# Kernel tuning notes

Hardware: AMD Instinct MI355X
Metric: run time of the kernel (lower is better)

The kernel has to match this reference:

```python
import jax, jax.numpy as jnp
import numpy as np

N = 100000
E = 1600000
F_IN = 128
DIM = 32
C = 2
BN_EPS = 1e-5


def setup_inputs() -> dict:
    key = jax.random.key(0)
    ks = jax.random.split(key, 24)
    s = 0.1
    inp = {
        'x': jax.random.normal(ks[0], (N, F_IN), dtype=jnp.float32),
        'edge_index': jax.random.randint(ks[1], (2, E), 0, N, dtype=jnp.int64),
        'edge_attr': jax.random.normal(ks[2], (E, 1), dtype=jnp.float32),
        'batch': jnp.zeros((N,), dtype=jnp.int64),
        # GIN layer 1 MLP: Linear(F_IN, DIM) -> ReLU -> Linear(DIM, DIM)
        'w1a': jax.random.normal(ks[3], (F_IN, DIM), dtype=jnp.float32) * s,
        'b1a': jnp.zeros((DIM,), dtype=jnp.float32),
        'w1b': jax.random.normal(ks[4], (DIM, DIM), dtype=jnp.float32) * s,
        'b1b': jnp.zeros((DIM,), dtype=jnp.float32),
        'g1': jnp.ones((DIM,), dtype=jnp.float32),
        'be1': jnp.zeros((DIM,), dtype=jnp.float32),
        # GIN layer 2
        'w2a': jax.random.normal(ks[5], (DIM, DIM), dtype=jnp.float32) * s,
        'b2a': jnp.zeros((DIM,), dtype=jnp.float32),
        'w2b': jax.random.normal(ks[6], (DIM, DIM), dtype=jnp.float32) * s,
        'b2b': jnp.zeros((DIM,), dtype=jnp.float32),
        'g2': jnp.ones((DIM,), dtype=jnp.float32),
        'be2': jnp.zeros((DIM,), dtype=jnp.float32),
        # GIN layer 3
        'w3a': jax.random.normal(ks[7], (DIM, DIM), dtype=jnp.float32) * s,
        'b3a': jnp.zeros((DIM,), dtype=jnp.float32),
        'w3b': jax.random.normal(ks[8], (DIM, DIM), dtype=jnp.float32) * s,
        'b3b': jnp.zeros((DIM,), dtype=jnp.float32),
        'g3': jnp.ones((DIM,), dtype=jnp.float32),
        'be3': jnp.zeros((DIM,), dtype=jnp.float32),
        # head
        'fw1': jax.random.normal(ks[9], (DIM, DIM), dtype=jnp.float32) * s,
        'fb1': jnp.zeros((DIM,), dtype=jnp.float32),
        'fw2': jax.random.normal(ks[10], (DIM, C), dtype=jnp.float32) * s,
        'fb2': jnp.zeros((C,), dtype=jnp.float32),
    }
    return inp


def _gin(x, src, dst, wa, ba, wb, bb):
    # GINConv with eps=0: h_i = MLP((1+eps)*x_i + sum_{j->i} x_j)
    agg = jax.ops.segment_sum(x[src], dst, num_segments=N)
    h = x + agg
    h = jax.nn.relu(h @ wa + ba) @ wb + bb
    return h


def _bn(h, g, b):
    # BatchNorm1d with batch statistics (training-mode normalization)
    mu = h.mean(axis=0)
    var = h.var(axis=0)  # biased, matches torch normalization
    return (h - mu) * jax.lax.rsqrt(var + BN_EPS) * g + b


def reference(x, edge_index, edge_attr, batch,
              w1a, b1a, w1b, b1b, g1, be1,
              w2a, b2a, w2b, b2b, g2, be2,
              w3a, b3a, w3b, b3b, g3, be3,
              fw1, fb1, fw2, fb2):
    src, dst = edge_index[0], edge_index[1]
    h = _bn(jax.nn.relu(_gin(x, src, dst, w1a, b1a, w1b, b1b)), g1, be1)
    h = _bn(jax.nn.relu(_gin(h, src, dst, w2a, b2a, w2b, b2b)), g2, be2)
    h = _bn(jax.nn.relu(_gin(h, src, dst, w3a, b3a, w3b, b3b)), g3, be3)
    h = jax.nn.relu(h @ fw1 + fb1)
    # dropout treated as identity (eval mode / deterministic reference)
    return h @ fw2 + fb2
```

## Files before the change

kernel.cpp:

```cpp
#include <hip/hip_runtime.h>

#define NNODES 100000
#define NEDGES 1600000
#define FIN 128
#define DIM 32
#define BN_EPS 1e-5f
#define NB_TPN ((NNODES + 255) / 256)
#define NBUK ((NNODES + 255) >> 8)
#define CH 8192

__global__ void __launch_bounds__(256) k_proj1(const float* __restrict__ x,
                                               const float* __restrict__ w,
                                               float* __restrict__ z) {
    const int i = blockIdx.x * 256 + threadIdx.x;
    if (i >= NNODES) return;
    const float4* xp = reinterpret_cast<const float4*>(x + (size_t)i * FIN);
    float acc[DIM];
#pragma unroll
    for (int c = 0; c < DIM; ++c) acc[c] = 0.f;

    for (int k0 = 0; k0 < FIN; k0 += 32) {
        float a[32];
        float4 r[8];
#pragma unroll
        for (int q = 0; q < 8; ++q) r[q] = xp[k0 / 4 + q];
#pragma unroll
        for (int q = 0; q < 8; ++q) {
            a[q * 4 + 0] = r[q].x; a[q * 4 + 1] = r[q].y;
            a[q * 4 + 2] = r[q].z; a[q * 4 + 3] = r[q].w;
        }
#pragma unroll
        for (int kk = 0; kk < 32; ++kk) {
            const float tk = a[kk];
#pragma unroll
            for (int c = 0; c < DIM; ++c)
                acc[c] += tk * w[(k0 + kk) * DIM + c];
        }
    }
    float4* zp = reinterpret_cast<float4*>(z + (size_t)i * DIM);
#pragma unroll
    for (int q = 0; q < 8; ++q)
        zp[q] = make_float4(acc[q * 4], acc[q * 4 + 1], acc[q * 4 + 2], acc[q * 4 + 3]);
}

__global__ void k_bhist(const int* __restrict__ ei, int* __restrict__ bucketCnt) {
    __shared__ int cnt[NBUK];
    for (int i = threadIdx.x; i < NBUK; i += 256) cnt[i] = 0;
    __syncthreads();
    const int tid    = blockIdx.x * blockDim.x + threadIdx.x;
    const int stride = gridDim.x * blockDim.x;
    for (int e = tid; e < NEDGES; e += stride)
        atomicAdd(&cnt[ei[NEDGES + e] >> 8], 1);
    __syncthreads();
    for (int i = threadIdx.x; i < NBUK; i += 256)
        if (cnt[i]) atomicAdd(&bucketCnt[i], cnt[i]);
}

__global__ void k_bscan(const int* __restrict__ bucketCnt,
                        int* __restrict__ bbase, int* __restrict__ gcur) {
    __shared__ int sbuf[512];
    const int t = threadIdx.x;
    const int v = (t < NBUK) ? bucketCnt[t] : 0;
    sbuf[t] = v;
    __syncthreads();
    for (int off = 1; off < 512; off <<= 1) {
        const int u = (t >= off) ? sbuf[t - off] : 0;
        __syncthreads();
        sbuf[t] += u;
        __syncthreads();
    }
    if (t < NBUK) { const int ex = sbuf[t] - v; bbase[t] = ex; gcur[t] = ex; }
    if (t == 0) bbase[NBUK] = NEDGES;
}

__global__ void __launch_bounds__(256) k_bscatter(const int* __restrict__ ei,
                                                  int* __restrict__ gcur,
                                                  int2* __restrict__ bucketed) {
    __shared__ int cnt[NBUK];
    __shared__ int base[NBUK];
    const int start = blockIdx.x * CH;
    const int end   = min(start + CH, NEDGES);
    for (int i = threadIdx.x; i < NBUK; i += 256) cnt[i] = 0;
    __syncthreads();
    for (int e = start + threadIdx.x; e < end; e += 256)
        atomicAdd(&cnt[ei[NEDGES + e] >> 8], 1);
    __syncthreads();
    for (int i = threadIdx.x; i < NBUK; i += 256) {
        const int c = cnt[i];
        base[i] = c ? atomicAdd(&gcur[i], c) : 0;
        cnt[i] = 0;
    }
    __syncthreads();
    for (int e = start + threadIdx.x; e < end; e += 256) {
        const int s = ei[e];
        const int d = ei[NEDGES + e];
        const int b = d >> 8;
        const int p = atomicAdd(&cnt[b], 1);
        bucketed[base[b] + p] = make_int2(s, d);
    }
}

__global__ void __launch_bounds__(256) k_bfill(const int2* __restrict__ bucketed,
                                               const int* __restrict__ bbase,
                                               int* __restrict__ rowstart,
                                               int* __restrict__ deg,
                                               int* __restrict__ sorted_src) {
    __shared__ int dcnt[256], dsc[256], cur[256];
    const int b  = blockIdx.x;
    const int lo = bbase[b];
    const int hi = bbase[b + 1];
    const int n0 = b << 8;
    const int t  = threadIdx.x;
    dcnt[t] = 0;
    __syncthreads();
    for (int p = lo + t; p < hi; p += 256)
        atomicAdd(&dcnt[bucketed[p].y - n0], 1);
    __syncthreads();
    const int myc = dcnt[t];
    dsc[t] = myc;
    __syncthreads();
    for (int off = 1; off < 256; off <<= 1) {
        const int u = (t >= off) ? dsc[t - off] : 0;
        __syncthreads();
        dsc[t] += u;
        __syncthreads();
    }
    const int ex = dsc[t] - myc;
    const int node = n0 + t;
    if (node < NNODES) { rowstart[node] = lo + ex; deg[node] = myc; }
    dcnt[t] = ex;
    cur[t] = 0;
    __syncthreads();
    for (int p = lo + t; p < hi; p += 256) {
        const int2 sd = bucketed[p];
        const int dl = sd.y - n0;
        const int pos = atomicAdd(&cur[dl], 1);
        sorted_src[lo + dcnt[dl] + pos] = sd.x;
    }
}

__global__ void k_gather_t(const float* __restrict__ z,
                           const int* __restrict__ rowstart,
                           const int* __restrict__ deg,
                           const int* __restrict__ sorted_src,
                           const float* __restrict__ ba,
                           float* __restrict__ tbuf) {
    const int lane = threadIdx.x & 31;
    const int g    = lane >> 3;
    const int f4   = lane & 7;
    const float4 ba4 = reinterpret_cast<const float4*>(ba)[f4];
    const int hw  = (blockIdx.x * blockDim.x + threadIdx.x) >> 5;
    const int nhw = (gridDim.x * blockDim.x) >> 5;

    for (int i = hw; i < NNODES; i += nhw) {
        const int base = rowstart[i];
        const int cnt  = deg[i];
        float4 agg0 = make_float4(0.f, 0.f, 0.f, 0.f);
        float4 agg1 = make_float4(0.f, 0.f, 0.f, 0.f);
        for (int k0 = 0; k0 < cnt; k0 += 32) {
            int e = 0;
            if (k0 + lane < cnt) e = sorted_src[base + k0 + lane];
            const int m = min(32, cnt - k0);
            for (int j = 0; j < m; j += 8) {
                const int s0 = __shfl(e, j + g, 32);
                const int s1 = __shfl(e, j + 4 + g, 32);
                if (j + g < m) {
                    const float4 zv = *reinterpret_cast<const float4*>(&z[s0 * DIM + f4 * 4]);
                    agg0.x += zv.x; agg0.y += zv.y; agg0.z += zv.z; agg0.w += zv.w;
                }
                if (j + 4 + g < m) {
                    const float4 zv = *reinterpret_cast<const float4*>(&z[s1 * DIM + f4 * 4]);
                    agg1.x += zv.x; agg1.y += zv.y; agg1.z += zv.z; agg1.w += zv.w;
                }
            }
        }
        agg0.x += agg1.x; agg0.y += agg1.y; agg0.z += agg1.z; agg0.w += agg1.w;
#pragma unroll
        for (int mask = 8; mask <= 16; mask <<= 1) {
            agg0.x += __shfl_xor(agg0.x, mask, 32);
            agg0.y += __shfl_xor(agg0.y, mask, 32);
            agg0.z += __shfl_xor(agg0.z, mask, 32);
            agg0.w += __shfl_xor(agg0.w, mask, 32);
        }
        if (g == 0) {
            const float4 zi = *reinterpret_cast<const float4*>(&z[i * DIM + f4 * 4]);
            float4 t;
            t.x = fmaxf(zi.x + agg0.x + ba4.x, 0.f);
            t.y = fmaxf(zi.y + agg0.y + ba4.y, 0.f);
            t.z = fmaxf(zi.z + agg0.z + ba4.z, 0.f);
            t.w = fmaxf(zi.w + agg0.w + ba4.w, 0.f);
            *reinterpret_cast<float4*>(&tbuf[i * DIM + f4 * 4]) = t;
        }
    }
}

__global__ void __launch_bounds__(256) k_mlp2(float* __restrict__ hbuf,
                                              const float* __restrict__ wb,
                                              const float* __restrict__ bb,
                                              float* __restrict__ stats) {
    __shared__ float ssum[DIM], ssq[DIM];
    if (threadIdx.x < DIM) { ssum[threadIdx.x] = 0.f; ssq[threadIdx.x] = 0.f; }
    __syncthreads();

    const int i = blockIdx.x * 256 + threadIdx.x;
    const bool valid = i < NNODES;

    float a[DIM];
    if (valid) {
        const float4* tp = reinterpret_cast<const float4*>(hbuf + (size_t)i * DIM);
        float4 r[8];
#pragma unroll
        for (int q = 0; q < 8; ++q) r[q] = tp[q];
#pragma unroll
        for (int q = 0; q < 8; ++q) {
            a[q * 4 + 0] = r[q].x; a[q * 4 + 1] = r[q].y;
            a[q * 4 + 2] = r[q].z; a[q * 4 + 3] = r[q].w;
        }
    } else {
#pragma unroll
        for (int k = 0; k < DIM; ++k) a[k] = 0.f;
    }

    float acc[DIM];
#pragma unroll
    for (int c = 0; c < DIM; ++c) acc[c] = bb[c];
#pragma unroll
    for (int k = 0; k < DIM; ++k) {
        const float tk = a[k];
#pragma unroll
        for (int c = 0; c < DIM; ++c)
            acc[c] += tk * wb[k * DIM + c];
    }
#pragma unroll
    for (int c = 0; c < DIM; ++c) acc[c] = valid ? fmaxf(acc[c], 0.f) : 0.f;

    if (valid) {
        float4* hp = reinterpret_cast<float4*>(hbuf + (size_t)i * DIM);
#pragma unroll
        for (int q = 0; q < 8; ++q)
            hp[q] = make_float4(acc[q * 4], acc[q * 4 + 1], acc[q * 4 + 2], acc[q * 4 + 3]);
    }

    const int lane = threadIdx.x & 63;
    float lsum = 0.f, lsq = 0.f;
#pragma unroll
    for (int c = 0; c < DIM; ++c) {
        float v  = acc[c];
        float w2 = acc[c] * acc[c];
#pragma unroll
        for (int off = 1; off < 64; off <<= 1) {
            v  += __shfl_xor(v, off);
            w2 += __shfl_xor(w2, off);
        }
        if (lane == c) { lsum = v; lsq = w2; }
    }
    if (lane < DIM) {
        atomicAdd(&ssum[lane], lsum);
        atomicAdd(&ssq[lane], lsq);
    }
    __syncthreads();
    if (threadIdx.x < DIM) {
        atomicAdd(&stats[threadIdx.x],       ssum[threadIdx.x]);
        atomicAdd(&stats[DIM + threadIdx.x], ssq[threadIdx.x]);
    }
}

__global__ void __launch_bounds__(256) k_projbn(const float* __restrict__ h,
                                                const float* __restrict__ stats,
                                                const float* __restrict__ g,
                                                const float* __restrict__ be,
                                                const float* __restrict__ wa,
                                                float* __restrict__ z) {
    const int i = blockIdx.x * 256 + threadIdx.x;
    if (i >= NNODES) return;
    const float4* hp = reinterpret_cast<const float4*>(h + (size_t)i * DIM);
    float a[DIM];
    float4 r[8];
#pragma unroll
    for (int q = 0; q < 8; ++q) r[q] = hp[q];
#pragma unroll
    for (int q = 0; q < 8; ++q) {
        a[q * 4 + 0] = r[q].x; a[q * 4 + 1] = r[q].y;
        a[q * 4 + 2] = r[q].z; a[q * 4 + 3] = r[q].w;
    }
    float acc[DIM];
#pragma unroll
    for (int c = 0; c < DIM; ++c) acc[c] = 0.f;
#pragma unroll
    for (int k = 0; k < DIM; ++k) {
        const float mu  = stats[k] * (1.f / NNODES);
        const float var = stats[DIM + k] * (1.f / NNODES) - mu * mu;
        const float ss  = g[k] * rsqrtf(var + BN_EPS);
        const float st  = be[k] - mu * ss;
        const float tk  = a[k] * ss + st;
#pragma unroll
        for (int c = 0; c < DIM; ++c)
            acc[c] += tk * wa[k * DIM + c];
    }
    float4* zp = reinterpret_cast<float4*>(z + (size_t)i * DIM);
#pragma unroll
    for (int q = 0; q < 8; ++q)
        zp[q] = make_float4(acc[q * 4], acc[q * 4 + 1], acc[q * 4 + 2], acc[q * 4 + 3]);
}

__global__ void __launch_bounds__(256) k_head(const float* __restrict__ h,
                                              const float* __restrict__ stats,
                                              const float* __restrict__ g,
                                              const float* __restrict__ be,
                                              const float* __restrict__ fw1,
                                              const float* __restrict__ fb1,
                                              const float* __restrict__ fw2,
                                              const float* __restrict__ fb2,
                                              float* __restrict__ out) {
    const int i = blockIdx.x * 256 + threadIdx.x;
    if (i >= NNODES) return;
    const float4* hp = reinterpret_cast<const float4*>(h + (size_t)i * DIM);
    float a[DIM];
    float4 r[8];
#pragma unroll
    for (int q = 0; q < 8; ++q) r[q] = hp[q];
#pragma unroll
    for (int q = 0; q < 8; ++q) {
        a[q * 4 + 0] = r[q].x; a[q * 4 + 1] = r[q].y;
        a[q * 4 + 2] = r[q].z; a[q * 4 + 3] = r[q].w;
    }
    float acc[DIM];
#pragma unroll
    for (int c = 0; c < DIM; ++c) acc[c] = fb1[c];
#pragma unroll
    for (int k = 0; k < DIM; ++k) {
        const float mu  = stats[k] * (1.f / NNODES);
        const float var = stats[DIM + k] * (1.f / NNODES) - mu * mu;
        const float ss  = g[k] * rsqrtf(var + BN_EPS);
        const float st  = be[k] - mu * ss;
        const float tk  = a[k] * ss + st;
#pragma unroll
        for (int c = 0; c < DIM; ++c)
            acc[c] += tk * fw1[k * DIM + c];
    }
    float o0 = fb2[0], o1 = fb2[1];
#pragma unroll
    for (int c = 0; c < DIM; ++c) {
        const float u = fmaxf(acc[c], 0.f);
        o0 += u * fw2[c * 2 + 0];
        o1 += u * fw2[c * 2 + 1];
    }
    *reinterpret_cast<float2*>(&out[i * 2]) = make_float2(o0, o1);
}

extern "C" void kernel_launch(void* const* d_in, const int* in_sizes, int n_in,
                              void* d_out, int out_size, void* d_ws, size_t ws_size,
                              hipStream_t stream) {
    const float* x   = (const float*)d_in[0];
    const int*   ei  = (const int*)d_in[1];
    const float* w1a = (const float*)d_in[4];
    const float* b1a = (const float*)d_in[5];
    const float* w1b = (const float*)d_in[6];
    const float* b1b = (const float*)d_in[7];
    const float* g1  = (const float*)d_in[8];
    const float* be1 = (const float*)d_in[9];
    const float* w2a = (const float*)d_in[10];
    const float* b2a = (const float*)d_in[11];
    const float* w2b = (const float*)d_in[12];
    const float* b2b = (const float*)d_in[13];
    const float* g2  = (const float*)d_in[14];
    const float* be2 = (const float*)d_in[15];
    const float* w3a = (const float*)d_in[16];
    const float* b3a = (const float*)d_in[17];
    const float* w3b = (const float*)d_in[18];
    const float* b3b = (const float*)d_in[19];
    const float* g3  = (const float*)d_in[20];
    const float* be3 = (const float*)d_in[21];
    const float* fw1 = (const float*)d_in[22];
    const float* fb1 = (const float*)d_in[23];
    const float* fw2 = (const float*)d_in[24];
    const float* fb2 = (const float*)d_in[25];
    float* out = (float*)d_out;

    float* ws = (float*)d_ws;
    const size_t nf = (size_t)NNODES * DIM;
    float* z     = ws;
    float* h     = ws + nf;
    int2*  bucketed = (int2*)h;
    float* stats = ws + 2 * nf;
    int* rowstart   = (int*)(ws + 2 * nf + 192);
    int* deg        = rowstart + NNODES;
    int* sorted_src = deg + NNODES;
    int* bucketCnt  = sorted_src + NEDGES;
    int* bbase      = bucketCnt + NBUK;
    int* gcur       = bbase + NBUK + 1;

    const int TB = 256, NB_G = 2048;

    hipMemsetAsync(stats, 0, 3 * 64 * sizeof(float), stream);
    hipMemsetAsync(bucketCnt, 0, NBUK * sizeof(int), stream);

    k_bhist<<<512, TB, 0, stream>>>(ei, bucketCnt);
    k_bscan<<<1, 512, 0, stream>>>(bucketCnt, bbase, gcur);
    k_bscatter<<<(NEDGES + CH - 1) / CH, TB, 0, stream>>>(ei, gcur, bucketed);
    k_bfill<<<NBUK, TB, 0, stream>>>(bucketed, bbase, rowstart, deg, sorted_src);

    k_proj1<<<NB_TPN, TB, 0, stream>>>(x, w1a, z);
    k_gather_t<<<NB_G, TB, 0, stream>>>(z, rowstart, deg, sorted_src, b1a, h);
    k_mlp2<<<NB_TPN, TB, 0, stream>>>(h, w1b, b1b, stats + 0);
    k_projbn<<<NB_TPN, TB, 0, stream>>>(h, stats + 0, g1, be1, w2a, z);
    k_gather_t<<<NB_G, TB, 0, stream>>>(z, rowstart, deg, sorted_src, b2a, h);
    k_mlp2<<<NB_TPN, TB, 0, stream>>>(h, w2b, b2b, stats + 64);
    k_projbn<<<NB_TPN, TB, 0, stream>>>(h, stats + 64, g2, be2, w3a, z);
    k_gather_t<<<NB_G, TB, 0, stream>>>(z, rowstart, deg, sorted_src, b3a, h);
    k_mlp2<<<NB_TPN, TB, 0, stream>>>(h, w3b, b3b, stats + 128);
    k_head<<<NB_TPN, TB, 0, stream>>>(h, stats + 128, g3, be3,
                                      fw1, fb1, fw2, fb2, out);
}
```

Baseline: 350.3 us.

## Fuse gather with second MLP layer and BN stats, pack bucketed edges

Merges the neighbor gather kernel and the second linear layer with BN statistics into one kernel. Each half-wavefront computes one output column per lane via shuffles, so the intermediate t buffer is never written to or re-read from global memory. Edge bucketing now packs the source index and the local destination offset into a single int, halving that scratch traffic. The stats memset is folded into the scan kernel, and the per-node kernels move to 64-thread blocks, with proj1 loading the whole input row up front. The packing assumes node ids fit in 17 bits, and the fused kernel does a 32-step shuffle chain for every node.

```diff
diff --git a/kernel.cpp b/kernel.cpp
--- a/kernel.cpp
+++ b/kernel.cpp
@@ -5,36 +5,37 @@
 #define FIN 128
 #define DIM 32
 #define BN_EPS 1e-5f
-#define NB_TPN ((NNODES + 255) / 256)
 #define NBUK ((NNODES + 255) >> 8)
 #define CH 8192
 
-__global__ void __launch_bounds__(256) k_proj1(const float* __restrict__ x,
-                                               const float* __restrict__ w,
-                                               float* __restrict__ z) {
-    const int i = blockIdx.x * 256 + threadIdx.x;
+__global__ void __launch_bounds__(64) k_proj1(const float* __restrict__ x,
+                                              const float* __restrict__ w,
+                                              float* __restrict__ z) {
+    const int i = blockIdx.x * 64 + threadIdx.x;
     if (i >= NNODES) return;
     const float4* xp = reinterpret_cast<const float4*>(x + (size_t)i * FIN);
+    float4 r[32];
+#pragma unroll
+    for (int q = 0; q < 32; ++q) r[q] = xp[q];
+
     float acc[DIM];
 #pragma unroll
     for (int c = 0; c < DIM; ++c) acc[c] = 0.f;
 
-    for (int k0 = 0; k0 < FIN; k0 += 32) {
+#pragma unroll
+    for (int k0 = 0; k0 < 4; ++k0) {
         float a[32];
-        float4 r[8];
-#pragma unroll
-        for (int q = 0; q < 8; ++q) r[q] = xp[k0 / 4 + q];
 #pragma unroll
         for (int q = 0; q < 8; ++q) {
-            a[q * 4 + 0] = r[q].x; a[q * 4 + 1] = r[q].y;
-            a[q * 4 + 2] = r[q].z; a[q * 4 + 3] = r[q].w;
+            a[q * 4 + 0] = r[k0 * 8 + q].x; a[q * 4 + 1] = r[k0 * 8 + q].y;
+            a[q * 4 + 2] = r[k0 * 8 + q].z; a[q * 4 + 3] = r[k0 * 8 + q].w;
         }
 #pragma unroll
         for (int kk = 0; kk < 32; ++kk) {
             const float tk = a[kk];
 #pragma unroll
             for (int c = 0; c < DIM; ++c)
-                acc[c] += tk * w[(k0 + kk) * DIM + c];
+                acc[c] += tk * w[(k0 * 32 + kk) * DIM + c];
         }
     }
     float4* zp = reinterpret_cast<float4*>(z + (size_t)i * DIM);
@@ -57,9 +58,11 @@
 }
 
 __global__ void k_bscan(const int* __restrict__ bucketCnt,
-                        int* __restrict__ bbase, int* __restrict__ gcur) {
+                        int* __restrict__ bbase, int* __restrict__ gcur,
+                        float* __restrict__ stats) {
     __shared__ int sbuf[512];
     const int t = threadIdx.x;
+    if (t < 192) stats[t] = 0.f;
     const int v = (t < NBUK) ? bucketCnt[t] : 0;
     sbuf[t] = v;
     __syncthreads();
@@ -75,7 +78,7 @@
 
 __global__ void __launch_bounds__(256) k_bscatter(const int* __restrict__ ei,
                                                   int* __restrict__ gcur,
-                                                  int2* __restrict__ bucketed) {
+                                                  int* __restrict__ bucketed) {
     __shared__ int cnt[NBUK];
     __shared__ int base[NBUK];
     const int start = blockIdx.x * CH;
@@ -96,11 +99,11 @@
         const int d = ei[NEDGES + e];
         const int b = d >> 8;
         const int p = atomicAdd(&cnt[b], 1);
-        bucketed[base[b] + p] = make_int2(s, d);
-    }
-}
-
-__global__ void __launch_bounds__(256) k_bfill(const int2* __restrict__ bucketed,
+        bucketed[base[b] + p] = s | ((d & 255) << 17);
+    }
+}
+
+__global__ void __launch_bounds__(256) k_bfill(const int* __restrict__ bucketed,
                                                const int* __restrict__ bbase,
                                                int* __restrict__ rowstart,
                                                int* __restrict__ deg,
@@ -109,12 +112,11 @@
     const int b  = blockIdx.x;
     const int lo = bbase[b];
     const int hi = bbase[b + 1];
-    const int n0 = b << 8;
     const int t  = threadIdx.x;
     dcnt[t] = 0;
     __syncthreads();
     for (int p = lo + t; p < hi; p += 256)
-        atomicAdd(&dcnt[bucketed[p].y - n0], 1);
+        atomicAdd(&dcnt[bucketed[p] >> 17], 1);
     __syncthreads();
     const int myc = dcnt[t];
     dsc[t] = myc;
@@ -126,31 +128,44 @@
         __syncthreads();
     }
     const int ex = dsc[t] - myc;
-    const int node = n0 + t;
+    const int node = (b << 8) + t;
     if (node < NNODES) { rowstart[node] = lo + ex; deg[node] = myc; }
     dcnt[t] = ex;
     cur[t] = 0;
     __syncthreads();
     for (int p = lo + t; p < hi; p += 256) {
-        const int2 sd = bucketed[p];
-        const int dl = sd.y - n0;
+        const int v = bucketed[p];
+        const int dl = v >> 17;
         const int pos = atomicAdd(&cur[dl], 1);
-        sorted_src[lo + dcnt[dl] + pos] = sd.x;
-    }
-}
-
-__global__ void k_gather_t(const float* __restrict__ z,
-                           const int* __restrict__ rowstart,
-                           const int* __restrict__ deg,
-                           const int* __restrict__ sorted_src,
-                           const float* __restrict__ ba,
-                           float* __restrict__ tbuf) {
+        sorted_src[lo + dcnt[dl] + pos] = v & 0x1FFFF;
+    }
+}
+
+__global__ void k_gather_mlp(const float* __restrict__ z,
+                             const int* __restrict__ rowstart,
+                             const int* __restrict__ deg,
+                             const int* __restrict__ sorted_src,
+                             const float* __restrict__ ba,
+                             const float* __restrict__ wb,
+                             const float* __restrict__ bb,
+                             float* __restrict__ h,
+                             float* __restrict__ stats) {
+    __shared__ float ssum[DIM], ssq[DIM];
+    if (threadIdx.x < DIM) { ssum[threadIdx.x] = 0.f; ssq[threadIdx.x] = 0.f; }
+    __syncthreads();
+
     const int lane = threadIdx.x & 31;
     const int g    = lane >> 3;
     const int f4   = lane & 7;
     const float4 ba4 = reinterpret_cast<const float4*>(ba)[f4];
+    float wcol[DIM];
+#pragma unroll
+    for (int kk = 0; kk < DIM; ++kk) wcol[kk] = wb[kk * DIM + lane];
+    const float bbl = bb[lane];
+
     const int hw  = (blockIdx.x * blockDim.x + threadIdx.x) >> 5;
     const int nhw = (gridDim.x * blockDim.x) >> 5;
+    float lsum = 0.f, lsq = 0.f;
 
     for (int i = hw; i < NNODES; i += nhw) {
         const int base = rowstart[i];
@@ -182,82 +197,31 @@
             agg0.z += __shfl_xor(agg0.z, mask, 32);
             agg0.w += __shfl_xor(agg0.w, mask, 32);
         }
-        if (g == 0) {
-            const float4 zi = *reinterpret_cast<const float4*>(&z[i * DIM + f4 * 4]);
-            float4 t;
-            t.x = fmaxf(zi.x + agg0.x + ba4.x, 0.f);
-            t.y = fmaxf(zi.y + agg0.y + ba4.y, 0.f);
-            t.z = fmaxf(zi.z + agg0.z + ba4.z, 0.f);
-            t.w = fmaxf(zi.w + agg0.w + ba4.w, 0.f);
-            *reinterpret_cast<float4*>(&tbuf[i * DIM + f4 * 4]) = t;
-        }
-    }
-}
-
-__global__ void __launch_bounds__(256) k_mlp2(float* __restrict__ hbuf,
-                                              const float* __restrict__ wb,
-                                              const float* __restrict__ bb,
-                                              float* __restrict__ stats) {
-    __shared__ float ssum[DIM], ssq[DIM];
-    if (threadIdx.x < DIM) { ssum[threadIdx.x] = 0.f; ssq[threadIdx.x] = 0.f; }
-    __syncthreads();
-
-    const int i = blockIdx.x * 256 + threadIdx.x;
-    const bool valid = i < NNODES;
-
-    float a[DIM];
-    if (valid) {
-        const float4* tp = reinterpret_cast<const float4*>(hbuf + (size_t)i * DIM);
-        float4 r[8];
-#pragma unroll
-        for (int q = 0; q < 8; ++q) r[q] = tp[q];
-#pragma unroll
-        for (int q = 0; q < 8; ++q) {
-            a[q * 4 + 0] = r[q].x; a[q * 4 + 1] = r[q].y;
-            a[q * 4 + 2] = r[q].z; a[q * 4 + 3] = r[q].w;
-        }
-    } else {
-#pragma unroll
-        for (int k = 0; k < DIM; ++k) a[k] = 0.f;
-    }
-
-    float acc[DIM];
-#pragma unroll
-    for (int c = 0; c < DIM; ++c) acc[c] = bb[c];
-#pragma unroll
-    for (int k = 0; k < DIM; ++k) {
-        const float tk = a[k];
-#pragma unroll
-        for (int c = 0; c < DIM; ++c)
-            acc[c] += tk * wb[k * DIM + c];
-    }
-#pragma unroll
-    for (int c = 0; c < DIM; ++c) acc[c] = valid ? fmaxf(acc[c], 0.f) : 0.f;
-
-    if (valid) {
-        float4* hp = reinterpret_cast<float4*>(hbuf + (size_t)i * DIM);
-#pragma unroll
-        for (int q = 0; q < 8; ++q)
-            hp[q] = make_float4(acc[q * 4], acc[q * 4 + 1], acc[q * 4 + 2], acc[q * 4 + 3]);
-    }
-
-    const int lane = threadIdx.x & 63;
-    float lsum = 0.f, lsq = 0.f;
-#pragma unroll
-    for (int c = 0; c < DIM; ++c) {
-        float v  = acc[c];
-        float w2 = acc[c] * acc[c];
-#pragma unroll
-        for (int off = 1; off < 64; off <<= 1) {
-            v  += __shfl_xor(v, off);
-            w2 += __shfl_xor(w2, off);
-        }
-        if (lane == c) { lsum = v; lsq = w2; }
-    }
-    if (lane < DIM) {
-        atomicAdd(&ssum[lane], lsum);
-        atomicAdd(&ssq[lane], lsq);
-    }
+        const float4 zi = *reinterpret_cast<const float4*>(&z[i * DIM + f4 * 4]);
+        float4 t4;
+        t4.x = fmaxf(zi.x + agg0.x + ba4.x, 0.f);
+        t4.y = fmaxf(zi.y + agg0.y + ba4.y, 0.f);
+        t4.z = fmaxf(zi.z + agg0.z + ba4.z, 0.f);
+        t4.w = fmaxf(zi.w + agg0.w + ba4.w, 0.f);
+
+        float acc = bbl;
+#pragma unroll
+        for (int kk = 0; kk < DIM; ++kk) {
+            float tv;
+            if ((kk & 3) == 0) tv = t4.x;
+            else if ((kk & 3) == 1) tv = t4.y;
+            else if ((kk & 3) == 2) tv = t4.z;
+            else tv = t4.w;
+            const float tkk = __shfl(tv, kk >> 2, 32);
+            acc += tkk * wcol[kk];
+        }
+        acc = fmaxf(acc, 0.f);
+        h[i * DIM + lane] = acc;
+        lsum += acc;
+        lsq  += acc * acc;
+    }
+    atomicAdd(&ssum[lane], lsum);
+    atomicAdd(&ssq[lane], lsq);
     __syncthreads();
     if (threadIdx.x < DIM) {
         atomicAdd(&stats[threadIdx.x],       ssum[threadIdx.x]);
@@ -265,19 +229,19 @@
     }
 }
 
-__global__ void __launch_bounds__(256) k_projbn(const float* __restrict__ h,
-                                                const float* __restrict__ stats,
-                                                const float* __restrict__ g,
-                                                const float* __restrict__ be,
-                                                const float* __restrict__ wa,
-                                                float* __restrict__ z) {
-    const int i = blockIdx.x * 256 + threadIdx.x;
+__global__ void __launch_bounds__(64) k_projbn(const float* __restrict__ h,
+                                               const float* __restrict__ stats,
+                                               const float* __restrict__ g,
+                                               const float* __restrict__ be,
+                                               const float* __restrict__ wa,
+                                               float* __restrict__ z) {
+    const int i = blockIdx.x * 64 + threadIdx.x;
     if (i >= NNODES) return;
     const float4* hp = reinterpret_cast<const float4*>(h + (size_t)i * DIM);
+    float4 r[8];
+#pragma unroll
+    for (int q = 0; q < 8; ++q) r[q] = hp[q];
     float a[DIM];
-    float4 r[8];
-#pragma unroll
-    for (int q = 0; q < 8; ++q) r[q] = hp[q];
 #pragma unroll
     for (int q = 0; q < 8; ++q) {
         a[q * 4 + 0] = r[q].x; a[q * 4 + 1] = r[q].y;
@@ -303,22 +267,22 @@
         zp[q] = make_float4(acc[q * 4], acc[q * 4 + 1], acc[q * 4 + 2], acc[q * 4 + 3]);
 }
 
-__global__ void __launch_bounds__(256) k_head(const float* __restrict__ h,
-                                              const float* __restrict__ stats,
-                                              const float* __restrict__ g,
-                                              const float* __restrict__ be,
-                                              const float* __restrict__ fw1,
-                                              const float* __restrict__ fb1,
-                                              const float* __restrict__ fw2,
-                                              const float* __restrict__ fb2,
-                                              float* __restrict__ out) {
-    const int i = blockIdx.x * 256 + threadIdx.x;
+__global__ void __launch_bounds__(64) k_head(const float* __restrict__ h,
+                                             const float* __restrict__ stats,
+                                             const float* __restrict__ g,
+                                             const float* __restrict__ be,
+                                             const float* __restrict__ fw1,
+                                             const float* __restrict__ fb1,
+                                             const float* __restrict__ fw2,
+                                             const float* __restrict__ fb2,
+                                             float* __restrict__ out) {
+    const int i = blockIdx.x * 64 + threadIdx.x;
     if (i >= NNODES) return;
     const float4* hp = reinterpret_cast<const float4*>(h + (size_t)i * DIM);
+    float4 r[8];
+#pragma unroll
+    for (int q = 0; q < 8; ++q) r[q] = hp[q];
     float a[DIM];
-    float4 r[8];
-#pragma unroll
-    for (int q = 0; q < 8; ++q) r[q] = hp[q];
 #pragma unroll
     for (int q = 0; q < 8; ++q) {
         a[q * 4 + 0] = r[q].x; a[q * 4 + 1] = r[q].y;
@@ -381,7 +345,7 @@
     const size_t nf = (size_t)NNODES * DIM;
     float* z     = ws;
     float* h     = ws + nf;
-    int2*  bucketed = (int2*)h;
+    int*   bucketed = (int*)h;
     float* stats = ws + 2 * nf;
     int* rowstart   = (int*)(ws + 2 * nf + 192);
     int* deg        = rowstart + NNODES;
@@ -391,24 +355,24 @@
     int* gcur       = bbase + NBUK + 1;
 
     const int TB = 256, NB_G = 2048;
-
-    hipMemsetAsync(stats, 0, 3 * 64 * sizeof(float), stream);
+    const int NB_T64 = (NNODES + 63) / 64;
+
     hipMemsetAsync(bucketCnt, 0, NBUK * sizeof(int), stream);
 
     k_bhist<<<512, TB, 0, stream>>>(ei, bucketCnt);
-    k_bscan<<<1, 512, 0, stream>>>(bucketCnt, bbase, gcur);
+    k_bscan<<<1, 512, 0, stream>>>(bucketCnt, bbase, gcur, stats);
     k_bscatter<<<(NEDGES + CH - 1) / CH, TB, 0, stream>>>(ei, gcur, bucketed);
     k_bfill<<<NBUK, TB, 0, stream>>>(bucketed, bbase, rowstart, deg, sorted_src);
 
-    k_proj1<<<NB_TPN, TB, 0, stream>>>(x, w1a, z);
-    k_gather_t<<<NB_G, TB, 0, stream>>>(z, rowstart, deg, sorted_src, b1a, h);
-    k_mlp2<<<NB_TPN, TB, 0, stream>>>(h, w1b, b1b, stats + 0);
-    k_projbn<<<NB_TPN, TB, 0, stream>>>(h, stats + 0, g1, be1, w2a, z);
-    k_gather_t<<<NB_G, TB, 0, stream>>>(z, rowstart, deg, sorted_src, b2a, h);
-    k_mlp2<<<NB_TPN, TB, 0, stream>>>(h, w2b, b2b, stats + 64);
-    k_projbn<<<NB_TPN, TB, 0, stream>>>(h, stats + 64, g2, be2, w3a, z);
-    k_gather_t<<<NB_G, TB, 0, stream>>>(z, rowstart, deg, sorted_src, b3a, h);
-    k_mlp2<<<NB_TPN, TB, 0, stream>>>(h, w3b, b3b, stats + 128);
-    k_head<<<NB_TPN, TB, 0, stream>>>(h, stats + 128, g3, be3,
+    k_proj1<<<NB_T64, 64, 0, stream>>>(x, w1a, z);
+    k_gather_mlp<<<NB_G, TB, 0, stream>>>(z, rowstart, deg, sorted_src,
+                                          b1a, w1b, b1b, h, stats + 0);
+    k_projbn<<<NB_T64, 64, 0, stream>>>(h, stats + 0, g1, be1, w2a, z);
+    k_gather_mlp<<<NB_G, TB, 0, stream>>>(z, rowstart, deg, sorted_src,
+                                          b2a, w2b, b2b, h, stats + 64);
+    k_projbn<<<NB_T64, 64, 0, stream>>>(h, stats + 64, g2, be2, w3a, z);
+    k_gather_mlp<<<NB_G, TB, 0, stream>>>(z, rowstart, deg, sorted_src,
+                                          b3a, w3b, b3b, h, stats + 128);
+    k_head<<<NB_T64, 64, 0, stream>>>(h, stats + 128, g3, be3,
                                       fw1, fb1, fw2, fb2, out);
 }
```

Result: slower. 425.2 us (+21.4%).

## Store gathered projections in bf16, pack bucketed edges, retune proj1

Applied to the files above, without the earlier changes.

Projected node features that feed the edge gather are now written as bf16 pairs, which halves the bytes read per edge in the three gather passes. The gather kernel is reorganized so each lane loads 8 bf16 values (16 bytes), letting 8 edges be processed per half-wave step. Bucketed edges are packed into one int (source plus local destination), halving that intermediate's traffic. The stats memset is folded into the scan kernel, and k_proj1 now uses 64-thread blocks with all inputs loaded up front. The trade-off is reduced precision in the aggregated features and packing that assumes node ids fit in 17 bits.

```diff
diff --git a/kernel.cpp b/kernel.cpp
--- a/kernel.cpp
+++ b/kernel.cpp
@@ -5,42 +5,60 @@
 #define FIN 128
 #define DIM 32
 #define BN_EPS 1e-5f
-#define NB_TPN ((NNODES + 255) / 256)
 #define NBUK ((NNODES + 255) >> 8)
 #define CH 8192
 
-__global__ void __launch_bounds__(256) k_proj1(const float* __restrict__ x,
-                                               const float* __restrict__ w,
-                                               float* __restrict__ z) {
-    const int i = blockIdx.x * 256 + threadIdx.x;
+__device__ __forceinline__ unsigned int f2bf2(float a, float b) {
+    union { float f; unsigned int u; } ua, ub;
+    ua.f = a; ub.f = b;
+    const unsigned int ra = (ua.u + 0x7FFFu + ((ua.u >> 16) & 1u)) >> 16;
+    const unsigned int rb = (ub.u + 0x7FFFu + ((ub.u >> 16) & 1u)) >> 16;
+    return ra | (rb << 16);
+}
+__device__ __forceinline__ float bf_lo(unsigned int u) {
+    union { unsigned int u; float f; } c; c.u = u << 16; return c.f;
+}
+__device__ __forceinline__ float bf_hi(unsigned int u) {
+    union { unsigned int u; float f; } c; c.u = u & 0xFFFF0000u; return c.f;
+}
+
+__global__ void __launch_bounds__(64) k_proj1(const float* __restrict__ x,
+                                              const float* __restrict__ w,
+                                              unsigned int* __restrict__ zb) {
+    const int i = blockIdx.x * 64 + threadIdx.x;
     if (i >= NNODES) return;
     const float4* xp = reinterpret_cast<const float4*>(x + (size_t)i * FIN);
+    float4 r[32];
+#pragma unroll
+    for (int q = 0; q < 32; ++q) r[q] = xp[q];
+
     float acc[DIM];
 #pragma unroll
     for (int c = 0; c < DIM; ++c) acc[c] = 0.f;
 
-    for (int k0 = 0; k0 < FIN; k0 += 32) {
+#pragma unroll
+    for (int k0 = 0; k0 < 4; ++k0) {
         float a[32];
-        float4 r[8];
-#pragma unroll
-        for (int q = 0; q < 8; ++q) r[q] = xp[k0 / 4 + q];
 #pragma unroll
         for (int q = 0; q < 8; ++q) {
-            a[q * 4 + 0] = r[q].x; a[q * 4 + 1] = r[q].y;
-            a[q * 4 + 2] = r[q].z; a[q * 4 + 3] = r[q].w;
+            a[q * 4 + 0] = r[k0 * 8 + q].x; a[q * 4 + 1] = r[k0 * 8 + q].y;
+            a[q * 4 + 2] = r[k0 * 8 + q].z; a[q * 4 + 3] = r[k0 * 8 + q].w;
         }
 #pragma unroll
         for (int kk = 0; kk < 32; ++kk) {
             const float tk = a[kk];
 #pragma unroll
             for (int c = 0; c < DIM; ++c)
-                acc[c] += tk * w[(k0 + kk) * DIM + c];
-        }
-    }
-    float4* zp = reinterpret_cast<float4*>(z + (size_t)i * DIM);
-#pragma unroll
-    for (int q = 0; q < 8; ++q)
-        zp[q] = make_float4(acc[q * 4], acc[q * 4 + 1], acc[q * 4 + 2], acc[q * 4 + 3]);
+                acc[c] += tk * w[(k0 * 32 + kk) * DIM + c];
+        }
+    }
+    uint4* zp = reinterpret_cast<uint4*>(zb + (size_t)i * 16);
+#pragma unroll
+    for (int q = 0; q < 4; ++q)
+        zp[q] = make_uint4(f2bf2(acc[q * 8 + 0], acc[q * 8 + 1]),
+                           f2bf2(acc[q * 8 + 2], acc[q * 8 + 3]),
+                           f2bf2(acc[q * 8 + 4], acc[q * 8 + 5]),
+                           f2bf2(acc[q * 8 + 6], acc[q * 8 + 7]));
 }
 
 __global__ void k_bhist(const int* __restrict__ ei, int* __restrict__ bucketCnt) {
@@ -57,9 +75,11 @@
 }
 
 __global__ void k_bscan(const int* __restrict__ bucketCnt,
-                        int* __restrict__ bbase, int* __restrict__ gcur) {
+                        int* __restrict__ bbase, int* __restrict__ gcur,
+                        float* __restrict__ stats) {
     __shared__ int sbuf[512];
     const int t = threadIdx.x;
+    if (t < 192) stats[t] = 0.f;
     const int v = (t < NBUK) ? bucketCnt[t] : 0;
     sbuf[t] = v;
     __syncthreads();
@@ -75,7 +95,7 @@
 
 __global__ void __launch_bounds__(256) k_bscatter(const int* __restrict__ ei,
                                                   int* __restrict__ gcur,
-                                                  int2* __restrict__ bucketed) {
+                                                  int* __restrict__ bucketed) {
     __shared__ int cnt[NBUK];
     __shared__ int base[NBUK];
     const int start = blockIdx.x * CH;
@@ -96,11 +116,11 @@
         const int d = ei[NEDGES + e];
         const int b = d >> 8;
         const int p = atomicAdd(&cnt[b], 1);
-        bucketed[base[b] + p] = make_int2(s, d);
-    }
-}
-
-__global__ void __launch_bounds__(256) k_bfill(const int2* __restrict__ bucketed,
+        bucketed[base[b] + p] = s | ((d & 255) << 17);
+    }
+}
+
+__global__ void __launch_bounds__(256) k_bfill(const int* __restrict__ bucketed,
                                                const int* __restrict__ bbase,
                                                int* __restrict__ rowstart,
                                                int* __restrict__ deg,
@@ -109,12 +129,11 @@
     const int b  = blockIdx.x;
     const int lo = bbase[b];
     const int hi = bbase[b + 1];
-    const int n0 = b << 8;
     const int t  = threadIdx.x;
     dcnt[t] = 0;
     __syncthreads();
     for (int p = lo + t; p < hi; p += 256)
-        atomicAdd(&dcnt[bucketed[p].y - n0], 1);
+        atomicAdd(&dcnt[bucketed[p] >> 17], 1);
     __syncthreads();
     const int myc = dcnt[t];
     dsc[t] = myc;
@@ -126,70 +145,79 @@
         __syncthreads();
     }
     const int ex = dsc[t] - myc;
-    const int node = n0 + t;
+    const int node = (b << 8) + t;
     if (node < NNODES) { rowstart[node] = lo + ex; deg[node] = myc; }
     dcnt[t] = ex;
     cur[t] = 0;
     __syncthreads();
     for (int p = lo + t; p < hi; p += 256) {
-        const int2 sd = bucketed[p];
-        const int dl = sd.y - n0;
+        const int v = bucketed[p];
+        const int dl = v >> 17;
         const int pos = atomicAdd(&cur[dl], 1);
-        sorted_src[lo + dcnt[dl] + pos] = sd.x;
-    }
-}
-
-__global__ void k_gather_t(const float* __restrict__ z,
+        sorted_src[lo + dcnt[dl] + pos] = v & 0x1FFFF;
+    }
+}
+
+__global__ void k_gather_t(const unsigned int* __restrict__ zb,
                            const int* __restrict__ rowstart,
                            const int* __restrict__ deg,
                            const int* __restrict__ sorted_src,
                            const float* __restrict__ ba,
                            float* __restrict__ tbuf) {
     const int lane = threadIdx.x & 31;
-    const int g    = lane >> 3;
-    const int f4   = lane & 7;
-    const float4 ba4 = reinterpret_cast<const float4*>(ba)[f4];
+    const int g    = lane >> 2;
+    const int q    = lane & 3;
+    const float4 baA = reinterpret_cast<const float4*>(ba)[q * 2];
+    const float4 baB = reinterpret_cast<const float4*>(ba)[q * 2 + 1];
+    const uint4* z4 = reinterpret_cast<const uint4*>(zb);
     const int hw  = (blockIdx.x * blockDim.x + threadIdx.x) >> 5;
     const int nhw = (gridDim.x * blockDim.x) >> 5;
 
     for (int i = hw; i < NNODES; i += nhw) {
         const int base = rowstart[i];
         const int cnt  = deg[i];
-        float4 agg0 = make_float4(0.f, 0.f, 0.f, 0.f);
-        float4 agg1 = make_float4(0.f, 0.f, 0.f, 0.f);
+        float4 aA = make_float4(0.f, 0.f, 0.f, 0.f);
+        float4 aB = make_float4(0.f, 0.f, 0.f, 0.f);
         for (int k0 = 0; k0 < cnt; k0 += 32) {
             int e = 0;
             if (k0 + lane < cnt) e = sorted_src[base + k0 + lane];
             const int m = min(32, cnt - k0);
             for (int j = 0; j < m; j += 8) {
-                const int s0 = __shfl(e, j + g, 32);
-                const int s1 = __shfl(e, j + 4 + g, 32);
+                const int src = __shfl(e, j + g, 32);
                 if (j + g < m) {
-                    const float4 zv = *reinterpret_cast<const float4*>(&z[s0 * DIM + f4 * 4]);
-                    agg0.x += zv.x; agg0.y += zv.y; agg0.z += zv.z; agg0.w += zv.w;
-                }
-                if (j + 4 + g < m) {
-                    const float4 zv = *reinterpret_cast<const float4*>(&z[s1 * DIM + f4 * 4]);
-                    agg1.x += zv.x; agg1.y += zv.y; agg1.z += zv.z; agg1.w += zv.w;
+                    const uint4 v = z4[src * 4 + q];
+                    aA.x += bf_lo(v.x); aA.y += bf_hi(v.x);
+                    aA.z += bf_lo(v.y); aA.w += bf_hi(v.y);
+                    aB.x += bf_lo(v.z); aB.y += bf_hi(v.z);
+                    aB.z += bf_lo(v.w); aB.w += bf_hi(v.w);
                 }
             }
         }
-        agg0.x += agg1.x; agg0.y += agg1.y; agg0.z += agg1.z; agg0.w += agg1.w;
-#pragma unroll
-        for (int mask = 8; mask <= 16; mask <<= 1) {
-            agg0.x += __shfl_xor(agg0.x, mask, 32);
-            agg0.y += __shfl_xor(agg0.y, mask, 32);
-            agg0.z += __shfl_xor(agg0.z, mask, 32);
-            agg0.w += __shfl_xor(agg0.w, mask, 32);
+#pragma unroll
+        for (int mask = 4; mask <= 16; mask <<= 1) {
+            aA.x += __shfl_xor(aA.x, mask, 32);
+            aA.y += __shfl_xor(aA.y, mask, 32);
+            aA.z += __shfl_xor(aA.z, mask, 32);
+            aA.w += __shfl_xor(aA.w, mask, 32);
+            aB.x += __shfl_xor(aB.x, mask, 32);
+            aB.y += __shfl_xor(aB.y, mask, 32);
+            aB.z += __shfl_xor(aB.z, mask, 32);
+            aB.w += __shfl_xor(aB.w, mask, 32);
         }
         if (g == 0) {
-            const float4 zi = *reinterpret_cast<const float4*>(&z[i * DIM + f4 * 4]);
-            float4 t;
-            t.x = fmaxf(zi.x + agg0.x + ba4.x, 0.f);
-            t.y = fmaxf(zi.y + agg0.y + ba4.y, 0.f);
-            t.z = fmaxf(zi.z + agg0.z + ba4.z, 0.f);
-            t.w = fmaxf(zi.w + agg0.w + ba4.w, 0.f);
-            *reinterpret_cast<float4*>(&tbuf[i * DIM + f4 * 4]) = t;
+            const uint4 v = z4[i * 4 + q];
+            float4 tA, tB;
+            tA.x = fmaxf(bf_lo(v.x) + aA.x + baA.x, 0.f);
+            tA.y = fmaxf(bf_hi(v.x) + aA.y + baA.y, 0.f);
+            tA.z = fmaxf(bf_lo(v.y) + aA.z + baA.z, 0.f);
+            tA.w = fmaxf(bf_hi(v.y) + aA.w + baA.w, 0.f);
+            tB.x = fmaxf(bf_lo(v.z) + aB.x + baB.x, 0.f);
+            tB.y = fmaxf(bf_hi(v.z) + aB.y + baB.y, 0.f);
+            tB.z = fmaxf(bf_lo(v.w) + aB.z + baB.z, 0.f);
+            tB.w = fmaxf(bf_hi(v.w) + aB.w + baB.w, 0.f);
+            float4* tp = reinterpret_cast<float4*>(tbuf + (size_t)i * DIM);
+            tp[q * 2 + 0] = tA;
+            tp[q * 2 + 1] = tB;
         }
     }
 }
@@ -210,11 +238,11 @@
         const float4* tp = reinterpret_cast<const float4*>(hbuf + (size_t)i * DIM);
         float4 r[8];
 #pragma unroll
-        for (int q = 0; q < 8; ++q) r[q] = tp[q];
-#pragma unroll
-        for (int q = 0; q < 8; ++q) {
-            a[q * 4 + 0] = r[q].x; a[q * 4 + 1] = r[q].y;
-            a[q * 4 + 2] = r[q].z; a[q * 4 + 3] = r[q].w;
+        for (int qq = 0; qq < 8; ++qq) r[qq] = tp[qq];
+#pragma unroll
+        for (int qq = 0; qq < 8; ++qq) {
+            a[qq * 4 + 0] = r[qq].x; a[qq * 4 + 1] = r[qq].y;
+            a[qq * 4 + 2] = r[qq].z; a[qq * 4 + 3] = r[qq].w;
         }
     } else {
 #pragma unroll
@@ -237,8 +265,8 @@
     if (valid) {
         float4* hp = reinterpret_cast<float4*>(hbuf + (size_t)i * DIM);
 #pragma unroll
-        for (int q = 0; q < 8; ++q)
-            hp[q] = make_float4(acc[q * 4], acc[q * 4 + 1], acc[q * 4 + 2], acc[q * 4 + 3]);
+        for (int qq = 0; qq < 8; ++qq)
+            hp[qq] = make_float4(acc[qq * 4], acc[qq * 4 + 1], acc[qq * 4 + 2], acc[qq * 4 + 3]);
     }
 
     const int lane = threadIdx.x & 63;
@@ -270,14 +298,14 @@
                                                 const float* __restrict__ g,
                                                 const float* __restrict__ be,
                                                 const float* __restrict__ wa,
-                                                float* __restrict__ z) {
+                                                unsigned int* __restrict__ zb) {
     const int i = blockIdx.x * 256 + threadIdx.x;
     if (i >= NNODES) return;
     const float4* hp = reinterpret_cast<const float4*>(h + (size_t)i * DIM);
+    float4 r[8];
+#pragma unroll
+    for (int q = 0; q < 8; ++q) r[q] = hp[q];
     float a[DIM];
-    float4 r[8];
-#pragma unroll
-    for (int q = 0; q < 8; ++q) r[q] = hp[q];
 #pragma unroll
     for (int q = 0; q < 8; ++q) {
         a[q * 4 + 0] = r[q].x; a[q * 4 + 1] = r[q].y;
@@ -297,10 +325,13 @@
         for (int c = 0; c < DIM; ++c)
             acc[c] += tk * wa[k * DIM + c];
     }
-    float4* zp = reinterpret_cast<float4*>(z + (size_t)i * DIM);
-#pragma unroll
-    for (int q = 0; q < 8; ++q)
-        zp[q] = make_float4(acc[q * 4], acc[q * 4 + 1], acc[q * 4 + 2], acc[q * 4 + 3]);
+    uint4* zp = reinterpret_cast<uint4*>(zb + (size_t)i * 16);
+#pragma unroll
+    for (int q = 0; q < 4; ++q)
+        zp[q] = make_uint4(f2bf2(acc[q * 8 + 0], acc[q * 8 + 1]),
+                           f2bf2(acc[q * 8 + 2], acc[q * 8 + 3]),
+                           f2bf2(acc[q * 8 + 4], acc[q * 8 + 5]),
+                           f2bf2(acc[q * 8 + 6], acc[q * 8 + 7]));
 }
 
 __global__ void __launch_bounds__(256) k_head(const float* __restrict__ h,
@@ -315,10 +346,10 @@
     const int i = blockIdx.x * 256 + threadIdx.x;
     if (i >= NNODES) return;
     const float4* hp = reinterpret_cast<const float4*>(h + (size_t)i * DIM);
+    float4 r[8];
+#pragma unroll
+    for (int q = 0; q < 8; ++q) r[q] = hp[q];
     float a[DIM];
-    float4 r[8];
-#pragma unroll
-    for (int q = 0; q < 8; ++q) r[q] = hp[q];
 #pragma unroll
     for (int q = 0; q < 8; ++q) {
         a[q * 4 + 0] = r[q].x; a[q * 4 + 1] = r[q].y;
@@ -365,12 +396,12 @@
     const float* b2b = (const float*)d_in[13];
     const float* g2  = (const float*)d_in[14];
     const float* be2 = (const float*)d_in[15];
+    const float* g3  = (const float*)d_in[20];
+    const float* be3 = (const float*)d_in[21];
     const float* w3a = (const float*)d_in[16];
     const float* b3a = (const float*)d_in[17];
     const float* w3b = (const float*)d_in[18];
     const float* b3b = (const float*)d_in[19];
-    const float* g3  = (const float*)d_in[20];
-    const float* be3 = (const float*)d_in[21];
     const float* fw1 = (const float*)d_in[22];
     const float* fb1 = (const float*)d_in[23];
     const float* fw2 = (const float*)d_in[24];
@@ -379,9 +410,9 @@
 
     float* ws = (float*)d_ws;
     const size_t nf = (size_t)NNODES * DIM;
-    float* z     = ws;
+    unsigned int* zb = (unsigned int*)ws;
     float* h     = ws + nf;
-    int2*  bucketed = (int2*)h;
+    int*   bucketed = (int*)h;
     float* stats = ws + 2 * nf;
     int* rowstart   = (int*)(ws + 2 * nf + 192);
     int* deg        = rowstart + NNODES;
@@ -391,23 +422,24 @@
     int* gcur       = bbase + NBUK + 1;
 
     const int TB = 256, NB_G = 2048;
-
-    hipMemsetAsync(stats, 0, 3 * 64 * sizeof(float), stream);
+    const int NB_TPN = (NNODES + 255) / 256;
+    const int NB_P1  = (NNODES + 63) / 64;
+
     hipMemsetAsync(bucketCnt, 0, NBUK * sizeof(int), stream);
 
     k_bhist<<<512, TB, 0, stream>>>(ei, bucketCnt);
-    k_bscan<<<1, 512, 0, stream>>>(bucketCnt, bbase, gcur);
+    k_bscan<<<1, 512, 0, stream>>>(bucketCnt, bbase, gcur, stats);
     k_bscatter<<<(NEDGES + CH - 1) / CH, TB, 0, stream>>>(ei, gcur, bucketed);
     k_bfill<<<NBUK, TB, 0, stream>>>(bucketed, bbase, rowstart, deg, sorted_src);
 
-    k_proj1<<<NB_TPN, TB, 0, stream>>>(x, w1a, z);
-    k_gather_t<<<NB_G, TB, 0, stream>>>(z, rowstart, deg, sorted_src, b1a, h);
+    k_proj1<<<NB_P1, 64, 0, stream>>>(x, w1a, zb);
+    k_gather_t<<<NB_G, TB, 0, stream>>>(zb, rowstart, deg, sorted_src, b1a, h);
     k_mlp2<<<NB_TPN, TB, 0, stream>>>(h, w1b, b1b, stats + 0);
-    k_projbn<<<NB_TPN, TB, 0, stream>>>(h, stats + 0, g1, be1, w2a, z);
-    k_gather_t<<<NB_G, TB, 0, stream>>>(z, rowstart, deg, sorted_src, b2a, h);
+    k_projbn<<<NB_TPN, TB, 0, stream>>>(h, stats + 0, g1, be1, w2a, zb);
+    k_gather_t<<<NB_G, TB, 0, stream>>>(zb, rowstart, deg, sorted_src, b2a, h);
     k_mlp2<<<NB_TPN, TB, 0, stream>>>(h, w2b, b2b, stats + 64);
-    k_projbn<<<NB_TPN, TB, 0, stream>>>(h, stats + 64, g2, be2, w3a, z);
-    k_gather_t<<<NB_G, TB, 0, stream>>>(z, rowstart, deg, sorted_src, b3a, h);
+    k_projbn<<<NB_TPN, TB, 0, stream>>>(h, stats + 64, g2, be2, w3a, zb);
+    k_gather_t<<<NB_G, TB, 0, stream>>>(zb, rowstart, deg, sorted_src, b3a, h);
     k_mlp2<<<NB_TPN, TB, 0, stream>>>(h, w3b, b3b, stats + 128);
     k_head<<<NB_TPN, TB, 0, stream>>>(h, stats + 128, g3, be3,
                                       fw1, fb1, fw2, fb2, out);
```

Result: slower. 379.6 us (+8.3%).
